# Kernel optimization log

Hardware: AMD Instinct MI355X
Metric: run time of the kernel (lower is better)

The kernel has to match this reference:

```python
import jax, jax.numpy as jnp
import numpy as np

D_MODEL = 1024
N_HEADS = 16
D_K = D_MODEL // N_HEADS
B, S = 4, 2048


def _xavier(key, out_dim, in_dim):
    limit = float(np.sqrt(6.0 / (in_dim + out_dim)))
    return jax.random.uniform(key, (out_dim, in_dim), jnp.float32, -limit, limit)


def setup_inputs() -> dict:
    key = jax.random.key(0)
    ks = jax.random.split(key, 7)
    return {
        "query": jax.random.normal(ks[0], (B, S, D_MODEL), jnp.float32),
        "key": jax.random.normal(ks[1], (B, S, D_MODEL), jnp.float32),
        "value": jax.random.normal(ks[2], (B, S, D_MODEL), jnp.float32),
        "W_q": _xavier(ks[3], D_MODEL, D_MODEL), "b_q": jnp.zeros((D_MODEL,), jnp.float32),
        "W_k": _xavier(ks[4], D_MODEL, D_MODEL), "b_k": jnp.zeros((D_MODEL,), jnp.float32),
        "W_v": _xavier(ks[5], D_MODEL, D_MODEL), "b_v": jnp.zeros((D_MODEL,), jnp.float32),
        "W_o": _xavier(ks[6], D_MODEL, D_MODEL), "b_o": jnp.zeros((D_MODEL,), jnp.float32),
    }


def reference(query, key, value, W_q, b_q, W_k, b_k, W_v, b_v, W_o, b_o):
    b, sq, _ = query.shape
    sk = key.shape[1]
    # Linear projections (torch Linear: x @ W.T + b), then split heads -> (b, h, s, d_k)
    Q = (query @ W_q.T + b_q).reshape(b, sq, N_HEADS, D_K).transpose(0, 2, 1, 3)
    K = (key @ W_k.T + b_k).reshape(b, sk, N_HEADS, D_K).transpose(0, 2, 1, 3)
    V = (value @ W_v.T + b_v).reshape(b, sk, N_HEADS, D_K).transpose(0, 2, 1, 3)
    # Naive full-score attention: (b, h, sq, sk) materialized, as in the original
    scores = jnp.einsum("bhqd,bhkd->bhqk", Q, K) / jnp.sqrt(jnp.float32(D_K))
    attn = jax.nn.softmax(scores, axis=-1)
    out = jnp.einsum("bhqk,bhkd->bhqd", attn, V)
    out = out.transpose(0, 2, 1, 3).reshape(b, sq, D_MODEL)
    return out @ W_o.T + b_o
```

## Files before the change

kernel.cpp:

```cpp
#include <hip/hip_runtime.h>
#include <hip/hip_bf16.h>
#include <cstdint>
#include <cstddef>

typedef unsigned short u16;
typedef unsigned int u32;
typedef __attribute__((ext_vector_type(8))) short bf16x8;
typedef __attribute__((ext_vector_type(4))) float f32x4;
typedef __attribute__((ext_vector_type(16))) float f32x16;
typedef __attribute__((ext_vector_type(4))) unsigned int u32x4;
typedef __attribute__((ext_vector_type(4))) unsigned short u16x4;

#define MFMA16(A,B,C) __builtin_amdgcn_mfma_f32_16x16x32_bf16(A,B,C,0,0,0)
#define MFMA32(A,B,C) __builtin_amdgcn_mfma_f32_32x32x16_bf16(A,B,C,0,0,0)

__device__ __forceinline__ u16 f2bf(float x) {
  __hip_bfloat16 h = __float2bfloat16(x);
  return __builtin_bit_cast(u16, h);
}

__device__ __forceinline__ float fast_exp2(float x) {
  float r;
  asm("v_exp_f32 %0, %1" : "=v"(r) : "v"(x));
  return r;
}

__device__ __forceinline__ void async_copy16(u16* lds, const u16* g) {
  __builtin_amdgcn_global_load_lds(
      (const __attribute__((address_space(1))) void*)g,
      (__attribute__((address_space(3))) void*)lds, 16, 0, 0);
}

__global__ void cvt4_kernel(const float* __restrict__ i0, const float* __restrict__ i1,
                            const float* __restrict__ i2, const float* __restrict__ i3,
                            u16* __restrict__ o0, u16* __restrict__ o1,
                            u16* __restrict__ o2, u16* __restrict__ o3, int n4) {
  const float* in; u16* out;
  switch (blockIdx.y) {
    case 0:  in = i0; out = o0; break;
    case 1:  in = i1; out = o1; break;
    case 2:  in = i2; out = o2; break;
    default: in = i3; out = o3; break;
  }
  int i = blockIdx.x * blockDim.x + threadIdx.x;
  int stride = gridDim.x * blockDim.x;
  for (; i < n4; i += stride) {
    float4 v = reinterpret_cast<const float4*>(in)[i];
    u16x4 o;
    o.x = f2bf(v.x); o.y = f2bf(v.y); o.z = f2bf(v.z); o.w = f2bf(v.w);
    reinterpret_cast<u16x4*>(out)[i] = o;
  }
}

template<bool BF16OUT>
__global__ __launch_bounds__(256, 2)
void gemm_nt_bias(const u16* __restrict__ A, const u16* __restrict__ W,
                  const float* __restrict__ bias, void* __restrict__ Cout,
                  int M, int N, int K, float scale) {
  __shared__ __attribute__((aligned(16))) u16 As[128*32];
  __shared__ __attribute__((aligned(16))) u16 Bs[128*32];
  const int t = threadIdx.x;
  const int lane = t & 63, wid = t >> 6;
  const int wr = wid >> 1, wc = wid & 1;
  const int g = lane >> 4, qc = lane & 15;
  const size_t m0 = (size_t)blockIdx.x * 128;
  const size_t n0 = (size_t)blockIdx.y * 128;
  f32x4 acc[4][4] = {};

  for (int k0 = 0; k0 < K; k0 += 32) {
    __syncthreads();
    #pragma unroll
    for (int c = 0; c < 2; ++c) {
      int s = c*256 + t;
      int row = s >> 2, ch = s & 3;
      int sch = ch ^ ((row >> 1) & 3);
      async_copy16(&As[s*8], &A[(m0 + row)*K + k0 + sch*8]);
    }
    #pragma unroll
    for (int c = 0; c < 2; ++c) {
      int s = c*256 + t;
      int row = s >> 2, ch = s & 3;
      int sch = ch ^ ((row >> 1) & 3);
      async_copy16(&Bs[s*8], &W[(n0 + row)*K + k0 + sch*8]);
    }
    __syncthreads();
    bf16x8 af[4], bfr[4];
    #pragma unroll
    for (int i = 0; i < 4; ++i) {
      int r = wr*64 + i*16 + qc;
      int ch = g ^ ((r >> 1) & 3);
      af[i] = *reinterpret_cast<const bf16x8*>(&As[r*32 + ch*8]);
    }
    #pragma unroll
    for (int j = 0; j < 4; ++j) {
      int r = wc*64 + j*16 + qc;
      int ch = g ^ ((r >> 1) & 3);
      bfr[j] = *reinterpret_cast<const bf16x8*>(&Bs[r*32 + ch*8]);
    }
    #pragma unroll
    for (int i = 0; i < 4; ++i)
      #pragma unroll
      for (int j = 0; j < 4; ++j)
        acc[i][j] = MFMA16(af[i], bfr[j], acc[i][j]);
  }

  #pragma unroll
  for (int j = 0; j < 4; ++j) {
    size_t col = n0 + wc*64 + j*16 + qc;
    float bv = bias[col];
    #pragma unroll
    for (int i = 0; i < 4; ++i) {
      #pragma unroll
      for (int r = 0; r < 4; ++r) {
        size_t row = m0 + wr*64 + i*16 + g*4 + r;
        float v = (acc[i][j][r] + bv) * scale;
        if (BF16OUT) ((u16*)Cout)[row*N + col] = f2bf(v);
        else         ((float*)Cout)[row*N + col] = v;
      }
    }
  }
}

__global__ __launch_bounds__(512, 4)
void flash_attn3(const u16* __restrict__ Qp, const u16* __restrict__ Kp,
                 const u16* __restrict__ Vp, u16* __restrict__ O) {
  __shared__ __attribute__((aligned(16))) u16 Ks[2][64*64];
  __shared__ __attribute__((aligned(16))) u16 Vt[3][64*64];
  const int t = threadIdx.x;
  const int w = t >> 6, lane = t & 63;
  const int l31 = lane & 31, hi = lane >> 5;
  const int bh = blockIdx.x;
  const size_t rowbase = (size_t)(bh >> 4) * 2048;
  const int hoff = (bh & 15) * 64;
  const int q0 = blockIdx.y * 256 + w * 32;
  const float THR = 11.5415603f;

  bf16x8 bq[4];
  {
    const u16* qp = &Qp[(rowbase + q0 + l31) * 1024 + hoff + hi * 8];
    #pragma unroll
    for (int dd = 0; dd < 4; ++dd) bq[dd] = *reinterpret_cast<const bf16x8*>(qp + dd*16);
  }

  f32x16 accO[2] = {};
  float m_run = 0.f, l_run = 0.f;
  u32 pwp[2][8];

  const int kvr_s = t >> 3, c_s = t & 7;
  const int sc_s = c_s ^ ((kvr_s >> 3) & 7);
  const int vd0_s = (t & 7) * 8;
  const int vcs = kvr_s >> 3;

  async_copy16(&Ks[0][t*8], &Kp[(rowbase + kvr_s)*1024 + hoff + sc_s*8]);
  bf16x8 vreg = *reinterpret_cast<const bf16x8*>(&Vp[(rowbase + kvr_s)*1024 + hoff + vd0_s]);

  int wi = 0, ri = 2;
  for (int kv = 0; kv < 32; ++kv) {
    const int kb = kv & 1;
    u16* vw = &Vt[0][0] + wi*4096;
    const u16* vrd = &Vt[0][0] + ri*4096;

    #pragma unroll
    for (int j = 0; j < 8; ++j) {
      int d = vd0_s + j;
      vw[d*64 + ((vcs ^ ((d>>3)&7))*8) + (kvr_s & 7)] = (u16)vreg[j];
    }
    __syncthreads();
    if (kv < 31) {
      const size_t nb = rowbase + (size_t)(kv+1)*64;
      async_copy16(&Ks[kb^1][t*8], &Kp[(nb + kvr_s)*1024 + hoff + sc_s*8]);
      vreg = *reinterpret_cast<const bf16x8*>(&Vp[(nb + kvr_s)*1024 + hoff + vd0_s]);
    }

    f32x16 sacc[2];
    {
      const float negm = -m_run;
      #pragma unroll
      for (int i = 0; i < 16; ++i) { sacc[0][i] = negm; sacc[1][i] = negm; }
    }
    #pragma unroll
    for (int n = 0; n < 2; ++n) {
      int kvr = n*32 + l31;
      int swz = (kvr >> 3) & 7;
      #pragma unroll
      for (int dd = 0; dd < 4; ++dd) {
        int ch = (2*dd + hi) ^ swz;
        bf16x8 ak = *reinterpret_cast<const bf16x8*>(&Ks[kb][kvr*64 + ch*8]);
        sacc[n] = MFMA32(ak, bq[dd], sacc[n]);
      }
    }

    if (kv > 0) {
      #pragma unroll
      for (int ks = 0; ks < 4; ++ks) {
        const int n = ks >> 1, kp = ks & 1;
        u32 wA0 = pwp[n][4*kp+0], wA1 = pwp[n][4*kp+1];
        u32 wB0 = pwp[n][4*kp+2], wB1 = pwp[n][4*kp+3];
        u32 s0 = hi ? wA0 : wB0, s1 = hi ? wA1 : wB1;
        u32 r0 = (u32)__shfl_xor((int)s0, 32);
        u32 r1 = (u32)__shfl_xor((int)s1, 32);
        u32 k0 = hi ? wB0 : wA0, k1 = hi ? wB1 : wA1;
        u32x4 fu;
        fu.x = hi ? r0 : k0; fu.y = hi ? r1 : k1;
        fu.z = hi ? k0 : r0; fu.w = hi ? k1 : r1;
        bf16x8 pa = __builtin_bit_cast(bf16x8, fu);
        #pragma unroll
        for (int dt = 0; dt < 2; ++dt) {
          int d = dt*32 + l31;
          int ch = (2*ks + hi) ^ ((d>>3)&7);
          bf16x8 bv = *reinterpret_cast<const bf16x8*>(&vrd[d*64 + ch*8]);
          accO[dt] = MFMA32(pa, bv, accO[dt]);
        }
      }
    }

    float a0 = fmaxf(fmaxf(sacc[0][0],sacc[0][1]),sacc[0][2]);
    float a1 = fmaxf(fmaxf(sacc[0][3],sacc[0][4]),sacc[0][5]);
    float a2 = fmaxf(fmaxf(sacc[0][6],sacc[0][7]),sacc[0][8]);
    float a3 = fmaxf(fmaxf(sacc[0][9],sacc[0][10]),sacc[0][11]);
    float a4 = fmaxf(fmaxf(sacc[0][12],sacc[0][13]),sacc[0][14]);
    float a5 = fmaxf(fmaxf(sacc[0][15],sacc[1][0]),sacc[1][1]);
    float a6 = fmaxf(fmaxf(sacc[1][2],sacc[1][3]),sacc[1][4]);
    float a7 = fmaxf(fmaxf(sacc[1][5],sacc[1][6]),sacc[1][7]);
    float a8 = fmaxf(fmaxf(sacc[1][8],sacc[1][9]),sacc[1][10]);
    float a9 = fmaxf(fmaxf(sacc[1][11],sacc[1][12]),sacc[1][13]);
    float aA = fmaxf(sacc[1][14],sacc[1][15]);
    float b0 = fmaxf(fmaxf(a0,a1),a2);
    float b1 = fmaxf(fmaxf(a3,a4),a5);
    float b2 = fmaxf(fmaxf(a6,a7),a8);
    float b3 = fmaxf(a9,aA);
    float mloc = fmaxf(fmaxf(b0,b1),fmaxf(b2,b3));
    float mx = fmaxf(mloc, __shfl_xor(mloc, 32));

    if (__any(mx > THR)) {
      float dm = fmaxf(mx, 0.f);
      float alpha = fast_exp2(-dm);
      m_run += dm;
      l_run *= alpha;
      #pragma unroll
      for (int n = 0; n < 2; ++n)
        #pragma unroll
        for (int r = 0; r < 16; ++r) sacc[n][r] -= dm;
      #pragma unroll
      for (int r = 0; r < 16; ++r) {
        int qrow = (r&3) + 8*(r>>2) + 4*hi;
        float ar = __shfl(alpha, qrow);
        accO[0][r] *= ar; accO[1][r] *= ar;
      }
    }

    #pragma unroll
    for (int n = 0; n < 2; ++n)
      #pragma unroll
      for (int r = 0; r < 16; ++r) sacc[n][r] = fast_exp2(sacc[n][r]);
    #pragma unroll
    for (int n = 0; n < 2; ++n)
      #pragma unroll
      for (int i = 0; i < 8; ++i)
        pwp[n][i] = (u32)f2bf(sacc[n][2*i]) | ((u32)f2bf(sacc[n][2*i+1]) << 16);
    float ts[16];
    #pragma unroll
    for (int i = 0; i < 16; ++i) ts[i] = sacc[0][i] + sacc[1][i];
    #pragma unroll
    for (int off = 8; off >= 1; off >>= 1)
      #pragma unroll
      for (int i = 0; i < off; ++i) ts[i] += ts[i + off];
    l_run += ts[0] + __shfl_xor(ts[0], 32);

    wi = (wi == 2) ? 0 : wi + 1;
    ri = (ri == 2) ? 0 : ri + 1;
  }

  {
    const u16* vrd = &Vt[0][0] + ri*4096;
    #pragma unroll
    for (int ks = 0; ks < 4; ++ks) {
      const int n = ks >> 1, kp = ks & 1;
      u32 wA0 = pwp[n][4*kp+0], wA1 = pwp[n][4*kp+1];
      u32 wB0 = pwp[n][4*kp+2], wB1 = pwp[n][4*kp+3];
      u32 s0 = hi ? wA0 : wB0, s1 = hi ? wA1 : wB1;
      u32 r0 = (u32)__shfl_xor((int)s0, 32);
      u32 r1 = (u32)__shfl_xor((int)s1, 32);
      u32 k0 = hi ? wB0 : wA0, k1 = hi ? wB1 : wA1;
      u32x4 fu;
      fu.x = hi ? r0 : k0; fu.y = hi ? r1 : k1;
      fu.z = hi ? k0 : r0; fu.w = hi ? k1 : r1;
      bf16x8 pa = __builtin_bit_cast(bf16x8, fu);
      #pragma unroll
      for (int dt = 0; dt < 2; ++dt) {
        int d = dt*32 + l31;
        int ch = (2*ks + hi) ^ ((d>>3)&7);
        bf16x8 bv = *reinterpret_cast<const bf16x8*>(&vrd[d*64 + ch*8]);
        accO[dt] = MFMA32(pa, bv, accO[dt]);
      }
    }
  }

  float linv = 1.0f / l_run;
  #pragma unroll
  for (int r = 0; r < 16; ++r) {
    int qrow = (r&3) + 8*(r>>2) + 4*hi;
    float lv = __shfl(linv, qrow);
    size_t orow = rowbase + q0 + qrow;
    O[orow*1024 + hoff + l31]      = f2bf(accO[0][r] * lv);
    O[orow*1024 + hoff + 32 + l31] = f2bf(accO[1][r] * lv);
  }
}

extern "C" void kernel_launch(void* const* d_in, const int* in_sizes, int n_in,
                              void* d_out, int out_size, void* d_ws, size_t ws_size,
                              hipStream_t stream) {
  (void)in_sizes; (void)n_in; (void)out_size; (void)ws_size;
  const float* query = (const float*)d_in[0];
  const float* key   = (const float*)d_in[1];
  const float* value = (const float*)d_in[2];
  const float* W_q   = (const float*)d_in[3];
  const float* b_q   = (const float*)d_in[4];
  const float* W_k   = (const float*)d_in[5];
  const float* b_k   = (const float*)d_in[6];
  const float* W_v   = (const float*)d_in[7];
  const float* b_v   = (const float*)d_in[8];
  const float* W_o   = (const float*)d_in[9];
  const float* b_o   = (const float*)d_in[10];

  const size_t sz_t = (size_t)8192 * 1024;
  const size_t sz_w = (size_t)1024 * 1024;
  u16* ws = (u16*)d_ws;
  u16* xq = ws;
  u16* xk = ws + 1*sz_t;
  u16* xv = ws + 2*sz_t;
  u16* Qp = ws + 3*sz_t;
  u16* Kp = ws + 4*sz_t;
  u16* Vp = ws + 5*sz_t;
  u16* wq = ws + 6*sz_t;
  u16* wk = wq + sz_w;
  u16* wv = wq + 2*sz_w;
  u16* wo = wq + 3*sz_w;

  const float SCL = 0.125f * 1.44269504089f;

  cvt4_kernel<<<dim3(512, 4), 256, 0, stream>>>(W_q, W_k, W_v, W_o,
                                                wq, wk, wv, wo, (int)(sz_w/4));
  cvt4_kernel<<<dim3(2048, 3), 256, 0, stream>>>(query, key, value, value,
                                                 xq, xk, xv, xv, (int)(sz_t/4));

  dim3 gg(8192/128, 1024/128);
  gemm_nt_bias<true><<<gg, 256, 0, stream>>>(xq, wq, b_q, Qp, 8192, 1024, 1024, SCL);
  gemm_nt_bias<true><<<gg, 256, 0, stream>>>(xk, wk, b_k, Kp, 8192, 1024, 1024, 1.0f);
  gemm_nt_bias<true><<<gg, 256, 0, stream>>>(xv, wv, b_v, Vp, 8192, 1024, 1024, 1.0f);

  flash_attn3<<<dim3(64, 8), 512, 0, stream>>>(Qp, Kp, Vp, xq);

  gemm_nt_bias<false><<<gg, 256, 0, stream>>>(xq, wo, b_o, d_out, 8192, 1024, 1024, 1.0f);
}
```

Before: 242.5 us.

## Double-buffer shared-memory tiles in projection GEMM to overlap loads with MFMA

The projection GEMM now keeps two LDS buffers for the A and W tiles. It issues the async global-to-LDS copies for the next K-step before computing on the current one, so the second barrier per iteration goes away. The goal is to hide global load latency behind the MFMA work. The cost is double the LDS footprint (32 KB per block). Overlap is only achieved if the compiler does not insert a full vmcnt wait before the LDS reads.

```diff
diff --git a/kernel.cpp b/kernel.cpp
--- a/kernel.cpp
+++ b/kernel.cpp
@@ -57,8 +57,8 @@
 void gemm_nt_bias(const u16* __restrict__ A, const u16* __restrict__ W,
                   const float* __restrict__ bias, void* __restrict__ Cout,
                   int M, int N, int K, float scale) {
-  __shared__ __attribute__((aligned(16))) u16 As[128*32];
-  __shared__ __attribute__((aligned(16))) u16 Bs[128*32];
+  __shared__ __attribute__((aligned(16))) u16 As[2][128*32];
+  __shared__ __attribute__((aligned(16))) u16 Bs[2][128*32];
   const int t = threadIdx.x;
   const int lane = t & 63, wid = t >> 6;
   const int wr = wid >> 1, wc = wid & 1;
@@ -67,42 +67,49 @@
   const size_t n0 = (size_t)blockIdx.y * 128;
   f32x4 acc[4][4] = {};
 
+#define GSTAGE(buf, k0_) do {                                         \
+    _Pragma("unroll")                                                 \
+    for (int c = 0; c < 2; ++c) {                                     \
+      int s = c*256 + t;                                              \
+      int row = s >> 2, ch = s & 3;                                   \
+      int sch = ch ^ ((row >> 1) & 3);                                \
+      async_copy16(&As[buf][s*8], &A[(m0 + row)*K + (k0_) + sch*8]);  \
+    }                                                                 \
+    _Pragma("unroll")                                                 \
+    for (int c = 0; c < 2; ++c) {                                     \
+      int s = c*256 + t;                                              \
+      int row = s >> 2, ch = s & 3;                                   \
+      int sch = ch ^ ((row >> 1) & 3);                                \
+      async_copy16(&Bs[buf][s*8], &W[(n0 + row)*K + (k0_) + sch*8]);  \
+    }                                                                 \
+  } while (0)
+
+  GSTAGE(0, 0);
+  int cur = 0;
   for (int k0 = 0; k0 < K; k0 += 32) {
     __syncthreads();
-    #pragma unroll
-    for (int c = 0; c < 2; ++c) {
-      int s = c*256 + t;
-      int row = s >> 2, ch = s & 3;
-      int sch = ch ^ ((row >> 1) & 3);
-      async_copy16(&As[s*8], &A[(m0 + row)*K + k0 + sch*8]);
-    }
-    #pragma unroll
-    for (int c = 0; c < 2; ++c) {
-      int s = c*256 + t;
-      int row = s >> 2, ch = s & 3;
-      int sch = ch ^ ((row >> 1) & 3);
-      async_copy16(&Bs[s*8], &W[(n0 + row)*K + k0 + sch*8]);
-    }
-    __syncthreads();
+    if (k0 + 32 < K) GSTAGE(cur ^ 1, k0 + 32);
     bf16x8 af[4], bfr[4];
     #pragma unroll
     for (int i = 0; i < 4; ++i) {
       int r = wr*64 + i*16 + qc;
       int ch = g ^ ((r >> 1) & 3);
-      af[i] = *reinterpret_cast<const bf16x8*>(&As[r*32 + ch*8]);
+      af[i] = *reinterpret_cast<const bf16x8*>(&As[cur][r*32 + ch*8]);
     }
     #pragma unroll
     for (int j = 0; j < 4; ++j) {
       int r = wc*64 + j*16 + qc;
       int ch = g ^ ((r >> 1) & 3);
-      bfr[j] = *reinterpret_cast<const bf16x8*>(&Bs[r*32 + ch*8]);
+      bfr[j] = *reinterpret_cast<const bf16x8*>(&Bs[cur][r*32 + ch*8]);
     }
     #pragma unroll
     for (int i = 0; i < 4; ++i)
       #pragma unroll
       for (int j = 0; j < 4; ++j)
         acc[i][j] = MFMA16(af[i], bfr[j], acc[i][j]);
-  }
+    cur ^= 1;
+  }
+#undef GSTAGE
 
   #pragma unroll
   for (int j = 0; j < 4; ++j) {
```

Result: no change. 244.5 us (+0.8%).
